# Performance work log

Hardware: AMD Instinct MI355X
Metric: run time of the kernel (lower is better)

## Reference

```python
import jax, jax.numpy as jnp
import numpy as np

B, D, NS, C, H = 4096, 1024, 16000, 1000, 256


def setup_inputs() -> dict:
    key = jax.random.key(0)
    ks = jax.random.split(key, 8)
    # L2-normalized image features (output of frozen CLIP encode_image + norm)
    q = jax.random.normal(ks[0], (B, D), jnp.float32)
    q = q / jnp.linalg.norm(q, axis=-1, keepdims=True)
    # zero-shot CLIP logits
    z = jax.random.normal(ks[1], (B, C), jnp.float32)
    # L2-normalized support/cache features
    keys = jax.random.normal(ks[2], (NS, D), jnp.float32)
    keys = keys / jnp.linalg.norm(keys, axis=-1, keepdims=True)
    # one-hot support labels
    labels = jax.random.randint(ks[3], (NS,), 0, C)
    values = jax.nn.one_hot(labels, C, dtype=jnp.float32)
    # gate MLP params (small init like nn.Linear default scale)
    fc1_w = jax.random.normal(ks[4], (H, D), jnp.float32) * 0.02
    fc1_b = jnp.zeros((H,), jnp.float32)
    fc2_w = jax.random.normal(ks[5], (2, H), jnp.float32) * 0.02
    fc2_b = jnp.zeros((2,), jnp.float32)
    post_scale = jnp.ones((1,), jnp.float32)
    return {"q": q, "z": z, "keys": keys, "values": values,
            "fc1_w": fc1_w, "fc1_b": fc1_b, "fc2_w": fc2_w, "fc2_b": fc2_b,
            "post_scale": post_scale}


def reference(q, z, keys, values, fc1_w, fc1_b, fc2_w, fc2_b, post_scale):
    # GateMLP: per-image alpha in (0,1), beta > 0
    x = jax.nn.relu(q @ fc1_w.T + fc1_b)            # [B, H]
    g = x @ fc2_w.T + fc2_b                          # [B, 2]
    alpha_hat = jax.nn.sigmoid(g[:, 0:1])            # [B, 1]
    beta = jax.nn.softplus(g[:, 1:2]) + 0.001        # [B, 1] (learn_beta=True)
    # cache logits: sim -> exp affinity -> label aggregation
    sim = q @ keys.T                                 # [B, Ns]
    affinity = jnp.exp(beta * sim)                   # [B, Ns]
    c = affinity @ values                            # [B, C]
    # gated convex fusion with zero-shot logits
    logits = ((1.0 - alpha_hat) * z + alpha_hat * c) * post_scale
    return (logits, alpha_hat, beta)
```

## Files before the change

kernel.cpp:

```cpp
#include <hip/hip_runtime.h>
#include <hip/hip_bf16.h>
#include <stdint.h>

#define B_  4096
#define D_  1024
#define NS_ 16000
#define C_  1000
#define H_  256
#define LBLK 4000
#define RSTRIDE 2048

typedef __attribute__((ext_vector_type(8))) short bf16x8;
typedef __attribute__((ext_vector_type(4))) float f32x4;
typedef __attribute__((ext_vector_type(16))) float f32x16;
typedef __attribute__((ext_vector_type(8))) int i32x8;

__device__ __forceinline__ unsigned short f2bf(float f) {
  union { float f; unsigned u; } v; v.f = f;
  unsigned u = v.u;
  u += 0x7FFF + ((u >> 16) & 1);
  return (unsigned short)(u >> 16);
}

__device__ __forceinline__ float bf2f(unsigned short h) {
  union { unsigned u; float f; } v; v.u = ((unsigned)h) << 16;
  return v.f;
}

__global__ void prep_kernel(const float4* __restrict__ q, const float4* __restrict__ keys,
                            const float4* __restrict__ fc1, const float* __restrict__ values,
                            ushort4* __restrict__ qb, int* __restrict__ q8,
                            int* __restrict__ keys8, ushort4* __restrict__ fc1b,
                            int* __restrict__ labels, int* __restrict__ hist) {
  if (blockIdx.x < LBLK) {
    const int s = blockIdx.x * 4 + (threadIdx.x >> 6);
    const int lane = threadIdx.x & 63;
    const float4* row = (const float4*)(values + (size_t)s * C_);
    int lab = -1;
    for (int j = lane; j < C_ / 4; j += 64) {
      float4 v = row[j];
      if (v.x > 0.5f) lab = j * 4 + 0;
      if (v.y > 0.5f) lab = j * 4 + 1;
      if (v.z > 0.5f) lab = j * 4 + 2;
      if (v.w > 0.5f) lab = j * 4 + 3;
      if (__ballot(lab >= 0)) break;
    }
    if (lab >= 0) { labels[s] = lab; atomicAdd(&hist[lab], 1); }
    return;
  }
  const size_t nq = (size_t)B_ * D_ / 4;
  const size_t nk = (size_t)NS_ * D_ / 4;
  const size_t nf = (size_t)H_ * D_ / 4;
  const size_t total = nq + nk + nf;
  const size_t nblk = gridDim.x - LBLK;
  for (size_t i = (blockIdx.x - LBLK) * (size_t)blockDim.x + threadIdx.x; i < total;
       i += nblk * blockDim.x) {
    if (i < nq) {
      float4 v = q[i];
      ushort4 r; r.x = f2bf(v.x); r.y = f2bf(v.y); r.z = f2bf(v.z); r.w = f2bf(v.w);
      qb[i] = r;
      int p = __builtin_amdgcn_cvt_pk_fp8_f32(v.x * 64.f, v.y * 64.f, 0, false);
      p     = __builtin_amdgcn_cvt_pk_fp8_f32(v.z * 64.f, v.w * 64.f, p, true);
      q8[i] = p;
    } else if (i < nq + nk) {
      size_t o = i - nq;
      float4 v = keys[o];
      int p = __builtin_amdgcn_cvt_pk_fp8_f32(v.x * 64.f, v.y * 64.f, 0, false);
      p     = __builtin_amdgcn_cvt_pk_fp8_f32(v.z * 64.f, v.w * 64.f, p, true);
      keys8[o] = p;
    } else {
      size_t o = i - nq - nk;
      float4 v = fc1[o];
      ushort4 r; r.x = f2bf(v.x); r.y = f2bf(v.y); r.z = f2bf(v.z); r.w = f2bf(v.w);
      fc1b[o] = r;
    }
  }
}

__global__ void scan_kernel(const int* __restrict__ hist, int* __restrict__ boff) {
  __shared__ int s[1024];
  const int t = threadIdx.x;
  int v = (t < C_) ? hist[t] : 0;
  s[t] = v; __syncthreads();
  for (int off = 1; off < 1024; off <<= 1) {
    int u = (t >= off) ? s[t - off] : 0;
    __syncthreads();
    s[t] += u;
    __syncthreads();
  }
  if (t == 0) boff[0] = 0;
  if (t < C_) boff[t + 1] = s[t];
}

__global__ void scatter_kernel(const int* __restrict__ labels, const int* __restrict__ boff,
                               int* __restrict__ cnt, int* __restrict__ sortidx,
                               int* __restrict__ labsorted) {
  const int sidx = blockIdx.x * blockDim.x + threadIdx.x;
  if (sidx >= NS_) return;
  const int lab = labels[sidx];
  const int pos = boff[lab] + atomicAdd(&cnt[lab], 1);
  sortidx[pos] = sidx;
  labsorted[pos] = lab;
}

__global__ void runid_kernel(const int* __restrict__ labsorted, int* __restrict__ runid) {
  __shared__ int s[1024];
  __shared__ int stile[126];
  const int t = threadIdx.x;
  const int c0 = t * 16;
  int flags[16];
  int cnt = 0;
  if (c0 < NS_) {
    int prev = (c0 == 0) ? labsorted[0] : labsorted[c0 - 1];
    #pragma unroll
    for (int i = 0; i < 16; ++i) {
      const int c = c0 + i;
      const int l = labsorted[c];
      const int f = (c != 0) && (l != prev);
      flags[i] = f; cnt += f; prev = l;
    }
  }
  s[t] = cnt; __syncthreads();
  for (int off = 1; off < 1024; off <<= 1) {
    int u = (t >= off) ? s[t - off] : 0;
    __syncthreads();
    s[t] += u;
    __syncthreads();
  }
  if (c0 < NS_ && (t & 7) == 0) stile[t >> 3] = (s[t] - cnt) + flags[0];
  __syncthreads();
  if (c0 < NS_) {
    int run = s[t] - cnt;
    const int tile = c0 >> 7;
    const int base = tile * 16 - stile[tile];
    #pragma unroll
    for (int i = 0; i < 16; ++i) { run += flags[i]; runid[c0 + i] = base + run; }
    if (c0 + 16 == NS_) runid[NS_] = (NS_ >> 7) * 16;
  }
}

__global__ void labstart_kernel(const int* __restrict__ boff, const int* __restrict__ runid,
                                int* __restrict__ labstart) {
  const int t = threadIdx.x;
  if (t <= C_) labstart[t] = runid[boff[t]];
}

template<int MODE>
__global__ __launch_bounds__(256, 2) void gemm_kernel(
    const short* __restrict__ A, const short* __restrict__ Bm,
    const float* __restrict__ bias, float* __restrict__ outp)
{
  __shared__ short As[128 * 64];
  __shared__ short Bs[128 * 64];

  const int tid  = threadIdx.x;
  const int wave = tid >> 6, lane = tid & 63;
  const int quad = lane >> 4, l16 = lane & 15;
  const int wm = wave >> 1, wn = wave & 1;
  const int rstart = blockIdx.x * 128;
  const int nstart = blockIdx.y * 128;

  f32x4 acc[4][4];
  #pragma unroll
  for (int i = 0; i < 4; ++i)
    #pragma unroll
    for (int j = 0; j < 4; ++j) acc[i][j] = (f32x4)0.f;

  const int r_  = (lane >> 3);
  const int kc_ = ((lane & 7) ^ r_) * 8;

  for (int kt = 0; kt < D_; kt += 64) {
    __syncthreads();
    #pragma unroll
    for (int i = 0; i < 4; ++i) {
      const int chunk = i * 4 + wave;
      const int r = chunk * 8 + r_;
      const short* gA = A  + (size_t)(rstart + r) * D_ + kt + kc_;
      const short* gB = Bm + (size_t)(nstart + r) * D_ + kt + kc_;
      __builtin_amdgcn_global_load_lds(
          (const __attribute__((address_space(1))) void*)gA,
          (__attribute__((address_space(3))) void*)(As + chunk * 512), 16, 0, 0);
      __builtin_amdgcn_global_load_lds(
          (const __attribute__((address_space(1))) void*)gB,
          (__attribute__((address_space(3))) void*)(Bs + chunk * 512), 16, 0, 0);
    }
    __syncthreads();
    #pragma unroll
    for (int ks = 0; ks < 64; ks += 32) {
      bf16x8 af[4], bfr[4];
      const int kb = (ks >> 3) + quad;
      #pragma unroll
      for (int mt = 0; mt < 4; ++mt) {
        const int row = wm * 64 + mt * 16 + l16;
        af[mt] = *(const bf16x8*)(As + row * 64 + ((kb ^ (row & 7)) << 3));
      }
      #pragma unroll
      for (int nt = 0; nt < 4; ++nt) {
        const int row = wn * 64 + nt * 16 + l16;
        bfr[nt] = *(const bf16x8*)(Bs + row * 64 + ((kb ^ (row & 7)) << 3));
      }
      #pragma unroll
      for (int mt = 0; mt < 4; ++mt)
        #pragma unroll
        for (int nt = 0; nt < 4; ++nt)
          acc[mt][nt] = __builtin_amdgcn_mfma_f32_16x16x32_bf16(af[mt], bfr[nt], acc[mt][nt], 0, 0, 0);
    }
  }

  #pragma unroll
  for (int mt = 0; mt < 4; ++mt) {
    const int rbase = wm * 64 + mt * 16 + quad * 4;
    #pragma unroll
    for (int nt = 0; nt < 4; ++nt) {
      const int cc = nstart + wn * 64 + nt * 16 + l16;
      const float bv = bias[cc];
      #pragma unroll
      for (int r = 0; r < 4; ++r) {
        float v = acc[mt][nt][r] + bv;
        outp[(size_t)(rstart + rbase + r) * H_ + cc] = v > 0.f ? v : 0.f;
      }
    }
  }
}

__device__ __forceinline__ i32x8 mx_frag(const char* base, int lrow, int kh, int sel) {
  const int c0 = kh * 4 + sel * 2;
  const int s = lrow & 7;
  const int4 lo = *(const int4*)(base + lrow * 128 + (((c0    ) ^ s) << 4));
  const int4 hi = *(const int4*)(base + lrow * 128 + (((c0 + 1) ^ s) << 4));
  i32x8 f;
  f[0] = lo.x; f[1] = lo.y; f[2] = lo.z; f[3] = lo.w;
  f[4] = hi.x; f[5] = hi.y; f[6] = hi.z; f[7] = hi.w;
  return f;
}

__global__ __launch_bounds__(256, 2) void mxgemm_kernel(
    const char* __restrict__ A8, const char* __restrict__ B8,
    const float* __restrict__ beta, float* __restrict__ partials,
    const int* __restrict__ sortidx, const int* __restrict__ runid)
{
  __shared__ __align__(16) char smem[32768];
  __shared__ float sbeta[128];
  __shared__ __align__(16) unsigned short Es[16 * 136];
  char* As = smem;
  char* Bs = smem + 16384;

  const int tid  = threadIdx.x;
  const int wave = tid >> 6, lane = tid & 63;
  const int sel  = lane >> 5, l32 = lane & 31;
  const int wm = wave >> 1, wn = wave & 1;
  const int rstart = blockIdx.x * 128;
  const int nstart = blockIdx.y * 128;

  for (int i = tid; i < (16 * 136) / 2; i += 256) ((int*)Es)[i] = 0;
  if (tid < 128) sbeta[tid] = beta[rstart + tid];
  __syncthreads();
  if (tid < 128) Es[(runid[nstart + tid] & 15) * 136 + tid] = 0x3F80;

  const int srow_ = (lane >> 3);
  const int gch_  = (lane & 7) ^ srow_;

  int arow[4], brow[4];
  #pragma unroll
  for (int i = 0; i < 4; ++i) {
    const int row = wave * 32 + i * 8 + srow_;
    arow[i] = rstart + row;
    brow[i] = sortidx[nstart + row];
  }

  f32x16 acc[2][2];
  #pragma unroll
  for (int i = 0; i < 2; ++i)
    #pragma unroll
    for (int j = 0; j < 2; ++j) acc[i][j] = (f32x16)0.f;

  for (int kt = 0; kt < D_; kt += 128) {
    __syncthreads();
    #pragma unroll
    for (int i = 0; i < 4; ++i) {
      const char* gA = A8 + (size_t)arow[i] * D_ + kt + (gch_ << 4);
      const char* gB = B8 + (size_t)brow[i] * D_ + kt + (gch_ << 4);
      __builtin_amdgcn_global_load_lds(
          (const __attribute__((address_space(1))) void*)gA,
          (__attribute__((address_space(3))) void*)(As + wave * 4096 + i * 1024), 16, 0, 0);
      __builtin_amdgcn_global_load_lds(
          (const __attribute__((address_space(1))) void*)gB,
          (__attribute__((address_space(3))) void*)(Bs + wave * 4096 + i * 1024), 16, 0, 0);
    }
    __syncthreads();
    #pragma unroll
    for (int kh = 0; kh < 2; ++kh) {
      i32x8 a0 = mx_frag(As, wm * 64 +  0 + l32, kh, sel);
      i32x8 a1 = mx_frag(As, wm * 64 + 32 + l32, kh, sel);
      i32x8 b0 = mx_frag(Bs, wn * 64 +  0 + l32, kh, sel);
      i32x8 b1 = mx_frag(Bs, wn * 64 + 32 + l32, kh, sel);
      acc[0][0] = __builtin_amdgcn_mfma_scale_f32_32x32x64_f8f6f4(a0, b0, acc[0][0], 0, 0, 0, 121, 0, 121);
      acc[0][1] = __builtin_amdgcn_mfma_scale_f32_32x32x64_f8f6f4(a0, b1, acc[0][1], 0, 0, 0, 121, 0, 121);
      acc[1][0] = __builtin_amdgcn_mfma_scale_f32_32x32x64_f8f6f4(a1, b0, acc[1][0], 0, 0, 0, 121, 0, 121);
      acc[1][1] = __builtin_amdgcn_mfma_scale_f32_32x32x64_f8f6f4(a1, b1, acc[1][1], 0, 0, 0, 121, 0, 121);
    }
  }

  __syncthreads();
  unsigned short* tile = (unsigned short*)smem;
  #pragma unroll
  for (int mt = 0; mt < 2; ++mt) {
    #pragma unroll
    for (int nt = 0; nt < 2; ++nt) {
      const int col = wn * 64 + nt * 32 + l32;
      const int cc = col >> 3, cl = col & 7;
      #pragma unroll
      for (int r = 0; r < 16; ++r) {
        const int row = wm * 64 + mt * 32 + (r & 3) + 8 * (r >> 2) + 4 * sel;
        const float v = __expf(sbeta[row] * acc[mt][nt][r]);
        tile[row * 128 + (((cc ^ (row & 7)) << 3) | cl)] = f2bf(v);
      }
    }
  }
  __syncthreads();

  {
    const int quad = lane >> 4, l16 = lane & 15;
    const int rowb = wave * 32;
    f32x4 racc[2];
    racc[0] = (f32x4)0.f; racc[1] = (f32x4)0.f;
    #pragma unroll
    for (int kc = 0; kc < 4; ++kc) {
      const bf16x8 bfrag = *(const bf16x8*)(Es + l16 * 136 + kc * 32 + quad * 8);
      #pragma unroll
      for (int rg = 0; rg < 2; ++rg) {
        const int row = rowb + rg * 16 + l16;
        const int kch = kc * 4 + quad;
        const bf16x8 afrag = *(const bf16x8*)(tile + row * 128 + ((kch ^ (row & 7)) << 3));
        racc[rg] = __builtin_amdgcn_mfma_f32_16x16x32_bf16(afrag, bfrag, racc[rg], 0, 0, 0);
      }
    }
    const int tb = (nstart >> 7) * 16;
    #pragma unroll
    for (int rg = 0; rg < 2; ++rg) {
      #pragma unroll
      for (int r = 0; r < 4; ++r) {
        const int row = rowb + rg * 16 + quad * 4 + r;
        partials[(size_t)(rstart + row) * RSTRIDE + tb + l16] = racc[rg][r];
      }
    }
  }
}

__global__ void gate_kernel(const float* __restrict__ x, const float* __restrict__ fc2_w,
                            const float* __restrict__ fc2_b, float* __restrict__ ab) {
  const int w = (int)((blockIdx.x * blockDim.x + threadIdx.x) >> 6);
  const int lane = threadIdx.x & 63;
  if (w >= B_) return;
  const float* xr = x + (size_t)w * H_;
  float g0 = 0.f, g1 = 0.f;
  #pragma unroll
  for (int j = 0; j < H_; j += 64) {
    float v = xr[j + lane];
    g0 += v * fc2_w[j + lane];
    g1 += v * fc2_w[H_ + j + lane];
  }
  #pragma unroll
  for (int off = 32; off > 0; off >>= 1) {
    g0 += __shfl_down(g0, off);
    g1 += __shfl_down(g1, off);
  }
  if (lane == 0) {
    g0 += fc2_b[0];
    g1 += fc2_b[1];
    ab[w]      = 1.f / (1.f + __expf(-g0));
    ab[B_ + w] = fmaxf(g1, 0.f) + log1pf(__expf(-fabsf(g1))) + 0.001f;
  }
}

__global__ __launch_bounds__(256) void reduce_kernel(
    const float* __restrict__ partials, const int* __restrict__ labstart,
    const float* __restrict__ z, const float* __restrict__ ps, float* __restrict__ out) {
  __shared__ float sp[RSTRIDE];
  __shared__ int sls[C_ + 1];
  const int b = blockIdx.x;
  const int t = threadIdx.x;
  for (int i = t; i <= C_; i += 256) sls[i] = labstart[i];
  __syncthreads();
  const int R = sls[C_];
  const float* prow = partials + (size_t)b * RSTRIDE;
  for (int i = t; i < R; i += 256) sp[i] = prow[i];
  __syncthreads();
  const float a  = out[(size_t)B_ * C_ + b];
  const float sc = ps[0];
  for (int lab = t; lab < C_; lab += 256) {
    float c = 0.f;
    for (int j = sls[lab]; j < sls[lab + 1]; ++j) c += sp[j];
    const size_t oi = (size_t)b * C_ + lab;
    out[oi] = ((1.f - a) * z[oi] + a * c) * sc;
  }
}

extern "C" void kernel_launch(void* const* d_in, const int* in_sizes, int n_in,
                              void* d_out, int out_size, void* d_ws, size_t ws_size,
                              hipStream_t stream) {
  const float* q          = (const float*)d_in[0];
  const float* z          = (const float*)d_in[1];
  const float* keys       = (const float*)d_in[2];
  const float* values     = (const float*)d_in[3];
  const float* fc1_w      = (const float*)d_in[4];
  const float* fc1_b      = (const float*)d_in[5];
  const float* fc2_w      = (const float*)d_in[6];
  const float* fc2_b      = (const float*)d_in[7];
  const float* post_scale = (const float*)d_in[8];
  float* out = (float*)d_out;

  char* ws = (char*)d_ws;
  short* qb        = (short*)(ws);
  char*  q8        = (char*) (ws +  8388608);
  char*  keys8     = (char*) (ws + 12582912);
  short* fc1b      = (short*)(ws + 28966912);
  int*   labels    = (int*)  (ws + 29491200);
  float* x         = (float*)(ws + 29555200);
  int*   hist      = (int*)  (ws + 33749504);
  int*   cnt       = (int*)  (ws + 33753600);
  int*   boff      = (int*)  (ws + 33757696);
  int*   sortidx   = (int*)  (ws + 33761792);
  int*   labsorted = (int*)  (ws + 33825792);
  int*   runid     = (int*)  (ws + 33889792);
  int*   labstart  = (int*)  (ws + 33953808);
  float* partials  = (float*)(ws + 33959936);

  float* alpha = out + (size_t)B_ * C_;
  float* beta  = alpha + B_;

  hipMemsetAsync(hist, 0, 8192, stream);

  prep_kernel<<<LBLK + 2048, 256, 0, stream>>>(
      (const float4*)q, (const float4*)keys, (const float4*)fc1_w, values,
      (ushort4*)qb, (int*)q8, (int*)keys8, (ushort4*)fc1b, labels, hist);

  scan_kernel<<<1, 1024, 0, stream>>>(hist, boff);
  scatter_kernel<<<(NS_ + 255) / 256, 256, 0, stream>>>(labels, boff, cnt, sortidx,
                                                        labsorted);
  runid_kernel<<<1, 1024, 0, stream>>>(labsorted, runid);
  labstart_kernel<<<1, 1024, 0, stream>>>(boff, runid, labstart);

  gemm_kernel<1><<<dim3(B_ / 128, H_ / 128), 256, 0, stream>>>(qb, fc1b, fc1_b, x);

  gate_kernel<<<(B_ * 64) / 256, 256, 0, stream>>>(x, fc2_w, fc2_b, alpha);

  mxgemm_kernel<<<dim3(B_ / 128, NS_ / 128), 256, 0, stream>>>(
      q8, keys8, beta, partials, sortidx, runid);

  reduce_kernel<<<B_, 256, 0, stream>>>(partials, labstart, z, post_scale, out);
}
```

Measured before the change: 331.7 us.

## Fuse label-sort kernels into one block and fuse fc1 GEMM with gate MLP

Merges the scan, scatter, run-id and label-start kernels into a single 1024-thread block that keeps boff, counts and sorted labels in shared memory. The fc1 GEMM is retiled to 32 rows by all 256 hidden columns per block, so the fc2 dot products, sigmoid and softplus are computed in the epilogue without writing the hidden activations to global memory. The prep kernel now gives each tensor its own range of blocks instead of one grid-stride loop with branches. This removes several launches and a global round trip, but the sort pipeline now runs on one block and the GEMM tile has less reuse of the A operand.

```diff
diff --git a/kernel.cpp b/kernel.cpp
--- a/kernel.cpp
+++ b/kernel.cpp
@@ -48,121 +48,117 @@
     if (lab >= 0) { labels[s] = lab; atomicAdd(&hist[lab], 1); }
     return;
   }
-  const size_t nq = (size_t)B_ * D_ / 4;
-  const size_t nk = (size_t)NS_ * D_ / 4;
-  const size_t nf = (size_t)H_ * D_ / 4;
-  const size_t total = nq + nk + nf;
-  const size_t nblk = gridDim.x - LBLK;
-  for (size_t i = (blockIdx.x - LBLK) * (size_t)blockDim.x + threadIdx.x; i < total;
-       i += nblk * blockDim.x) {
-    if (i < nq) {
+  const int cb = blockIdx.x - LBLK;
+  if (cb < 512) {
+    const size_t n = (size_t)B_ * D_ / 4;
+    for (size_t i = (size_t)cb * 256 + threadIdx.x; i < n; i += 512 * 256) {
       float4 v = q[i];
       ushort4 r; r.x = f2bf(v.x); r.y = f2bf(v.y); r.z = f2bf(v.z); r.w = f2bf(v.w);
       qb[i] = r;
       int p = __builtin_amdgcn_cvt_pk_fp8_f32(v.x * 64.f, v.y * 64.f, 0, false);
       p     = __builtin_amdgcn_cvt_pk_fp8_f32(v.z * 64.f, v.w * 64.f, p, true);
       q8[i] = p;
-    } else if (i < nq + nk) {
-      size_t o = i - nq;
-      float4 v = keys[o];
+    }
+  } else if (cb < 2560) {
+    const size_t n = (size_t)NS_ * D_ / 4;
+    for (size_t i = (size_t)(cb - 512) * 256 + threadIdx.x; i < n; i += 2048 * 256) {
+      float4 v = keys[i];
       int p = __builtin_amdgcn_cvt_pk_fp8_f32(v.x * 64.f, v.y * 64.f, 0, false);
       p     = __builtin_amdgcn_cvt_pk_fp8_f32(v.z * 64.f, v.w * 64.f, p, true);
-      keys8[o] = p;
-    } else {
-      size_t o = i - nq - nk;
-      float4 v = fc1[o];
+      keys8[i] = p;
+    }
+  } else {
+    const size_t n = (size_t)H_ * D_ / 4;
+    for (size_t i = (size_t)(cb - 2560) * 256 + threadIdx.x; i < n; i += 32 * 256) {
+      float4 v = fc1[i];
       ushort4 r; r.x = f2bf(v.x); r.y = f2bf(v.y); r.z = f2bf(v.z); r.w = f2bf(v.w);
-      fc1b[o] = r;
-    }
-  }
-}
-
-__global__ void scan_kernel(const int* __restrict__ hist, int* __restrict__ boff) {
-  __shared__ int s[1024];
+      fc1b[i] = r;
+    }
+  }
+}
+
+__global__ __launch_bounds__(1024) void sortpipe_kernel(
+    const int* __restrict__ hist, const int* __restrict__ labels,
+    int* __restrict__ sortidx, int* __restrict__ runid, int* __restrict__ labstart)
+{
+  __shared__ int sscan[1024];
+  __shared__ int sboff[C_ + 1];
+  __shared__ int scnt[C_];
+  __shared__ unsigned short slab[NS_];
+  __shared__ int stile[NS_ / 128];
   const int t = threadIdx.x;
+
   int v = (t < C_) ? hist[t] : 0;
-  s[t] = v; __syncthreads();
+  sscan[t] = v;
+  if (t < C_) scnt[t] = 0;
+  __syncthreads();
   for (int off = 1; off < 1024; off <<= 1) {
-    int u = (t >= off) ? s[t - off] : 0;
-    __syncthreads();
-    s[t] += u;
-    __syncthreads();
-  }
-  if (t == 0) boff[0] = 0;
-  if (t < C_) boff[t + 1] = s[t];
-}
-
-__global__ void scatter_kernel(const int* __restrict__ labels, const int* __restrict__ boff,
-                               int* __restrict__ cnt, int* __restrict__ sortidx,
-                               int* __restrict__ labsorted) {
-  const int sidx = blockIdx.x * blockDim.x + threadIdx.x;
-  if (sidx >= NS_) return;
-  const int lab = labels[sidx];
-  const int pos = boff[lab] + atomicAdd(&cnt[lab], 1);
-  sortidx[pos] = sidx;
-  labsorted[pos] = lab;
-}
-
-__global__ void runid_kernel(const int* __restrict__ labsorted, int* __restrict__ runid) {
-  __shared__ int s[1024];
-  __shared__ int stile[126];
-  const int t = threadIdx.x;
+    int u = (t >= off) ? sscan[t - off] : 0;
+    __syncthreads(); sscan[t] += u; __syncthreads();
+  }
+  if (t == 0) sboff[0] = 0;
+  if (t < C_) sboff[t + 1] = sscan[t];
+  __syncthreads();
+
+  for (int s = t; s < NS_; s += 1024) {
+    const int lab = labels[s];
+    const int pos = sboff[lab] + atomicAdd(&scnt[lab], 1);
+    sortidx[pos] = s;
+    slab[pos] = (unsigned short)lab;
+  }
+  __syncthreads();
+
   const int c0 = t * 16;
-  int flags[16];
-  int cnt = 0;
+  int flags[16]; int cnt = 0;
   if (c0 < NS_) {
-    int prev = (c0 == 0) ? labsorted[0] : labsorted[c0 - 1];
+    int prev = (c0 == 0) ? slab[0] : slab[c0 - 1];
     #pragma unroll
     for (int i = 0; i < 16; ++i) {
-      const int c = c0 + i;
-      const int l = labsorted[c];
-      const int f = (c != 0) && (l != prev);
+      const int l = slab[c0 + i];
+      const int f = ((c0 + i) != 0) && (l != prev);
       flags[i] = f; cnt += f; prev = l;
     }
   }
-  s[t] = cnt; __syncthreads();
+  sscan[t] = cnt; __syncthreads();
   for (int off = 1; off < 1024; off <<= 1) {
-    int u = (t >= off) ? s[t - off] : 0;
-    __syncthreads();
-    s[t] += u;
-    __syncthreads();
-  }
-  if (c0 < NS_ && (t & 7) == 0) stile[t >> 3] = (s[t] - cnt) + flags[0];
+    int u = (t >= off) ? sscan[t - off] : 0;
+    __syncthreads(); sscan[t] += u; __syncthreads();
+  }
+  if (c0 < NS_ && (t & 7) == 0) stile[t >> 3] = (sscan[t] - cnt) + flags[0];
   __syncthreads();
   if (c0 < NS_) {
-    int run = s[t] - cnt;
-    const int tile = c0 >> 7;
-    const int base = tile * 16 - stile[tile];
-    #pragma unroll
-    for (int i = 0; i < 16; ++i) { run += flags[i]; runid[c0 + i] = base + run; }
-    if (c0 + 16 == NS_) runid[NS_] = (NS_ >> 7) * 16;
-  }
-}
-
-__global__ void labstart_kernel(const int* __restrict__ boff, const int* __restrict__ runid,
-                                int* __restrict__ labstart) {
-  const int t = threadIdx.x;
-  if (t <= C_) labstart[t] = runid[boff[t]];
-}
-
-template<int MODE>
-__global__ __launch_bounds__(256, 2) void gemm_kernel(
+    int run = sscan[t] - cnt;
+    const int base = (c0 >> 7) * 16 - stile[c0 >> 7];
+    #pragma unroll
+    for (int i = 0; i < 16; ++i) {
+      run += flags[i];
+      runid[c0 + i] = base + run;
+    }
+  }
+  if (t == 0) runid[NS_] = (NS_ >> 7) * 16;
+  __threadfence();
+  __syncthreads();
+  if (t <= C_) labstart[t] = runid[sboff[t]];
+}
+
+__global__ __launch_bounds__(256, 2) void gemmgate_kernel(
     const short* __restrict__ A, const short* __restrict__ Bm,
-    const float* __restrict__ bias, float* __restrict__ outp)
+    const float* __restrict__ bias, const float* __restrict__ fc2_w,
+    const float* __restrict__ fc2_b, float* __restrict__ ab)
 {
-  __shared__ short As[128 * 64];
-  __shared__ short Bs[128 * 64];
+  __shared__ short As[32 * 64];
+  __shared__ short Bs[256 * 64];
+  __shared__ float gred[4][32][2];
 
   const int tid  = threadIdx.x;
   const int wave = tid >> 6, lane = tid & 63;
   const int quad = lane >> 4, l16 = lane & 15;
-  const int wm = wave >> 1, wn = wave & 1;
-  const int rstart = blockIdx.x * 128;
-  const int nstart = blockIdx.y * 128;
-
-  f32x4 acc[4][4];
-  #pragma unroll
-  for (int i = 0; i < 4; ++i)
+  const int wn = wave;
+  const int rstart = blockIdx.x * 32;
+
+  f32x4 acc[2][4];
+  #pragma unroll
+  for (int i = 0; i < 2; ++i)
     #pragma unroll
     for (int j = 0; j < 4; ++j) acc[i][j] = (f32x4)0.f;
 
@@ -171,27 +167,30 @@
 
   for (int kt = 0; kt < D_; kt += 64) {
     __syncthreads();
-    #pragma unroll
-    for (int i = 0; i < 4; ++i) {
-      const int chunk = i * 4 + wave;
-      const int r = chunk * 8 + r_;
-      const short* gA = A  + (size_t)(rstart + r) * D_ + kt + kc_;
-      const short* gB = Bm + (size_t)(nstart + r) * D_ + kt + kc_;
+    {
+      const int row = wave * 8 + r_;
+      const short* gA = A + (size_t)(rstart + row) * D_ + kt + kc_;
       __builtin_amdgcn_global_load_lds(
           (const __attribute__((address_space(1))) void*)gA,
-          (__attribute__((address_space(3))) void*)(As + chunk * 512), 16, 0, 0);
+          (__attribute__((address_space(3))) void*)(As + wave * 512), 16, 0, 0);
+    }
+    #pragma unroll
+    for (int i = 0; i < 8; ++i) {
+      const int g = i * 4 + wave;
+      const int row = g * 8 + r_;
+      const short* gB = Bm + (size_t)row * D_ + kt + kc_;
       __builtin_amdgcn_global_load_lds(
           (const __attribute__((address_space(1))) void*)gB,
-          (__attribute__((address_space(3))) void*)(Bs + chunk * 512), 16, 0, 0);
+          (__attribute__((address_space(3))) void*)(Bs + g * 512), 16, 0, 0);
     }
     __syncthreads();
     #pragma unroll
     for (int ks = 0; ks < 64; ks += 32) {
-      bf16x8 af[4], bfr[4];
+      bf16x8 af[2], bfr[4];
       const int kb = (ks >> 3) + quad;
       #pragma unroll
-      for (int mt = 0; mt < 4; ++mt) {
-        const int row = wm * 64 + mt * 16 + l16;
+      for (int mt = 0; mt < 2; ++mt) {
+        const int row = mt * 16 + l16;
         af[mt] = *(const bf16x8*)(As + row * 64 + ((kb ^ (row & 7)) << 3));
       }
       #pragma unroll
@@ -200,26 +199,55 @@
         bfr[nt] = *(const bf16x8*)(Bs + row * 64 + ((kb ^ (row & 7)) << 3));
       }
       #pragma unroll
-      for (int mt = 0; mt < 4; ++mt)
+      for (int mt = 0; mt < 2; ++mt)
         #pragma unroll
         for (int nt = 0; nt < 4; ++nt)
           acc[mt][nt] = __builtin_amdgcn_mfma_f32_16x16x32_bf16(af[mt], bfr[nt], acc[mt][nt], 0, 0, 0);
     }
   }
 
-  #pragma unroll
-  for (int mt = 0; mt < 4; ++mt) {
-    const int rbase = wm * 64 + mt * 16 + quad * 4;
-    #pragma unroll
-    for (int nt = 0; nt < 4; ++nt) {
-      const int cc = nstart + wn * 64 + nt * 16 + l16;
-      const float bv = bias[cc];
+  float g0p[2][4], g1p[2][4];
+  #pragma unroll
+  for (int mt = 0; mt < 2; ++mt)
+    #pragma unroll
+    for (int r = 0; r < 4; ++r) { g0p[mt][r] = 0.f; g1p[mt][r] = 0.f; }
+  #pragma unroll
+  for (int nt = 0; nt < 4; ++nt) {
+    const int col = wn * 64 + nt * 16 + l16;
+    const float bv = bias[col];
+    const float w0 = fc2_w[col], w1 = fc2_w[H_ + col];
+    #pragma unroll
+    for (int mt = 0; mt < 2; ++mt)
       #pragma unroll
       for (int r = 0; r < 4; ++r) {
-        float v = acc[mt][nt][r] + bv;
-        outp[(size_t)(rstart + rbase + r) * H_ + cc] = v > 0.f ? v : 0.f;
-      }
-    }
+        float xv = acc[mt][nt][r] + bv;
+        xv = xv > 0.f ? xv : 0.f;
+        g0p[mt][r] += xv * w0;
+        g1p[mt][r] += xv * w1;
+      }
+  }
+  #pragma unroll
+  for (int mt = 0; mt < 2; ++mt)
+    #pragma unroll
+    for (int r = 0; r < 4; ++r) {
+      float a0 = g0p[mt][r], a1 = g1p[mt][r];
+      #pragma unroll
+      for (int off = 8; off > 0; off >>= 1) {
+        a0 += __shfl_xor(a0, off);
+        a1 += __shfl_xor(a1, off);
+      }
+      if (l16 == 0) {
+        const int row = mt * 16 + quad * 4 + r;
+        gred[wave][row][0] = a0;
+        gred[wave][row][1] = a1;
+      }
+    }
+  __syncthreads();
+  if (tid < 32) {
+    float g0 = gred[0][tid][0] + gred[1][tid][0] + gred[2][tid][0] + gred[3][tid][0] + fc2_b[0];
+    float g1 = gred[0][tid][1] + gred[1][tid][1] + gred[2][tid][1] + gred[3][tid][1] + fc2_b[1];
+    ab[rstart + tid]      = 1.f / (1.f + __expf(-g0));
+    ab[B_ + rstart + tid] = fmaxf(g1, 0.f) + log1pf(__expf(-fabsf(g1))) + 0.001f;
   }
 }
 
@@ -344,32 +372,6 @@
         partials[(size_t)(rstart + row) * RSTRIDE + tb + l16] = racc[rg][r];
       }
     }
-  }
-}
-
-__global__ void gate_kernel(const float* __restrict__ x, const float* __restrict__ fc2_w,
-                            const float* __restrict__ fc2_b, float* __restrict__ ab) {
-  const int w = (int)((blockIdx.x * blockDim.x + threadIdx.x) >> 6);
-  const int lane = threadIdx.x & 63;
-  if (w >= B_) return;
-  const float* xr = x + (size_t)w * H_;
-  float g0 = 0.f, g1 = 0.f;
-  #pragma unroll
-  for (int j = 0; j < H_; j += 64) {
-    float v = xr[j + lane];
-    g0 += v * fc2_w[j + lane];
-    g1 += v * fc2_w[H_ + j + lane];
-  }
-  #pragma unroll
-  for (int off = 32; off > 0; off >>= 1) {
-    g0 += __shfl_down(g0, off);
-    g1 += __shfl_down(g1, off);
-  }
-  if (lane == 0) {
-    g0 += fc2_b[0];
-    g1 += fc2_b[1];
-    ab[w]      = 1.f / (1.f + __expf(-g0));
-    ab[B_ + w] = fmaxf(g1, 0.f) + log1pf(__expf(-fabsf(g1))) + 0.001f;
   }
 }
 
@@ -416,12 +418,8 @@
   char*  keys8     = (char*) (ws + 12582912);
   short* fc1b      = (short*)(ws + 28966912);
   int*   labels    = (int*)  (ws + 29491200);
-  float* x         = (float*)(ws + 29555200);
   int*   hist      = (int*)  (ws + 33749504);
-  int*   cnt       = (int*)  (ws + 33753600);
-  int*   boff      = (int*)  (ws + 33757696);
   int*   sortidx   = (int*)  (ws + 33761792);
-  int*   labsorted = (int*)  (ws + 33825792);
   int*   runid     = (int*)  (ws + 33889792);
   int*   labstart  = (int*)  (ws + 33953808);
   float* partials  = (float*)(ws + 33959936);
@@ -429,21 +427,15 @@
   float* alpha = out + (size_t)B_ * C_;
   float* beta  = alpha + B_;
 
-  hipMemsetAsync(hist, 0, 8192, stream);
-
-  prep_kernel<<<LBLK + 2048, 256, 0, stream>>>(
+  hipMemsetAsync(hist, 0, 4096, stream);
+
+  prep_kernel<<<LBLK + 2592, 256, 0, stream>>>(
       (const float4*)q, (const float4*)keys, (const float4*)fc1_w, values,
       (ushort4*)qb, (int*)q8, (int*)keys8, (ushort4*)fc1b, labels, hist);
 
-  scan_kernel<<<1, 1024, 0, stream>>>(hist, boff);
-  scatter_kernel<<<(NS_ + 255) / 256, 256, 0, stream>>>(labels, boff, cnt, sortidx,
-                                                        labsorted);
-  runid_kernel<<<1, 1024, 0, stream>>>(labsorted, runid);
-  labstart_kernel<<<1, 1024, 0, stream>>>(boff, runid, labstart);
-
-  gemm_kernel<1><<<dim3(B_ / 128, H_ / 128), 256, 0, stream>>>(qb, fc1b, fc1_b, x);
-
-  gate_kernel<<<(B_ * 64) / 256, 256, 0, stream>>>(x, fc2_w, fc2_b, alpha);
+  sortpipe_kernel<<<1, 1024, 0, stream>>>(hist, labels, sortidx, runid, labstart);
+
+  gemmgate_kernel<<<B_ / 32, 256, 0, stream>>>(qb, fc1b, fc1_b, fc2_w, fc2_b, alpha);
 
   mxgemm_kernel<<<dim3(B_ / 128, NS_ / 128), 256, 0, stream>>>(
       q8, keys8, beta, partials, sortidx, runid);
```

Result: no change. 328.6 us (-0.9%).
